# Kernel optimization log

Hardware: AMD Instinct MI355X
Metric: run time of the kernel (lower is better)

Reference implementation:

```python
import jax, jax.numpy as jnp
from jax import lax
import numpy as np

NODE = 100000
D = 256      # input_dim
H = 256      # hidden_dim
P = 4096     # num paths between the pair
L = 8        # path length (hops)
OUT = 1


def setup_inputs() -> dict:
    key = jax.random.key(0)
    ks = jax.random.split(key, 10)
    s = 1.0 / np.sqrt(H)
    return {
        "embedding": jax.random.normal(ks[0], (NODE, D), jnp.float32) * 0.1,
        "w_ih": jax.random.normal(ks[1], (4 * H, D), jnp.float32) * s,
        "w_hh": jax.random.normal(ks[2], (4 * H, H), jnp.float32) * s,
        "b_ih": jax.random.normal(ks[3], (4 * H,), jnp.float32) * s,
        "b_hh": jax.random.normal(ks[4], (4 * H,), jnp.float32) * s,
        "w_lin": jax.random.normal(ks[5], (OUT, H + 2 * D), jnp.float32) * 0.05,
        "b_lin": jax.random.normal(ks[6], (OUT,), jnp.float32) * 0.05,
        "paths": jax.random.randint(ks[7], (P, L), 0, NODE, jnp.int64),
        "user_id": jax.random.randint(ks[8], (1,), 0, NODE, jnp.int64),
        "item_id": jax.random.randint(ks[9], (1,), 0, NODE, jnp.int64),
    }


def _lstm_final_hidden(x, w_ih, w_hh, b_ih, b_hh):
    # x: [P, L, D] -> final hidden state h_n: [P, H] (PyTorch gate order i,f,g,o)
    p, _, _ = x.shape
    h = x.shape  # noqa (shape comment)
    hidden = w_hh.shape[1]
    b = b_ih + b_hh

    def step(carry, x_t):
        h, c = carry
        gates = x_t @ w_ih.T + h @ w_hh.T + b  # [P, 4H]
        i, f, g, o = jnp.split(gates, 4, axis=-1)
        c = jax.nn.sigmoid(f) * c + jax.nn.sigmoid(i) * jnp.tanh(g)
        h = jax.nn.sigmoid(o) * jnp.tanh(c)
        return (h, c), None

    h0 = jnp.zeros((p, hidden), x.dtype)
    c0 = jnp.zeros((p, hidden), x.dtype)
    (h_n, _), _ = lax.scan(step, (h0, c0), jnp.swapaxes(x, 0, 1))  # scan over L
    return h_n


def reference(embedding, w_ih, w_hh, b_ih, b_hh, w_lin, b_lin, paths, user_id, item_id):
    # Batched version of the per-path loop: embed all paths, one LSTM scan.
    x = embedding[paths]                                   # [P, L, D]
    sum_hidden = _lstm_final_hidden(x, w_ih, w_hh, b_ih, b_hh)  # [P, H] (== stacked h_n)

    # MaxPool2d((1, H)) over hidden dim -> attention logits over paths
    att = jnp.max(sum_hidden, axis=-1, keepdims=True)      # [P, 1]
    att = jax.nn.softmax(att, axis=0)                      # softmax over paths
    path_emb = jnp.sum(sum_hidden * att, axis=0, keepdims=True)  # [1, H]

    user_emb = embedding[user_id]                          # [1, D]
    item_emb = embedding[item_id]                          # [1, D]
    emb = jnp.concatenate([user_emb, item_emb, path_emb], axis=-1)  # [1, 2D+H]
    out = jax.nn.sigmoid(emb @ w_lin.T + b_lin)            # [1, OUT]
    return out
```

## Files before the change

kernel.cpp:

```cpp
#include <hip/hip_runtime.h>
#include <stdint.h>

#define NPATHS 4096
#define LPATH  8
#define DIM    256
#define HID    256

typedef short  short4v __attribute__((ext_vector_type(4)));
typedef short  short8v __attribute__((ext_vector_type(8)));
typedef float  float4v __attribute__((ext_vector_type(4)));

__device__ __forceinline__ unsigned short f2bf(float f) {
    union { float f; uint32_t u; } v; v.f = f;
    uint32_t u = v.u;
    u += 0x7FFFu + ((u >> 16) & 1u);
    return (unsigned short)(u >> 16);
}
__device__ __forceinline__ float bf2f(unsigned short s) {
    return __uint_as_float(((uint32_t)s) << 16);
}
__device__ __forceinline__ float fast_sigmoid(float x) {
    return 1.0f / (1.0f + __expf(-x));
}
__device__ __forceinline__ float fast_tanh(float x) {
    x = fminf(15.0f, fmaxf(-15.0f, x));
    float e = __expf(2.0f * x);
    return (e - 1.0f) / (e + 1.0f);
}

__device__ __forceinline__ void dma16(void* lds, const void* g) {
    typedef const unsigned int __attribute__((address_space(1)))* gp_t;
    typedef unsigned int __attribute__((address_space(3)))* lp_t;
    gp_t gp = reinterpret_cast<gp_t>(reinterpret_cast<uintptr_t>(g));
    lp_t lp = reinterpret_cast<lp_t>(static_cast<unsigned int>(reinterpret_cast<uintptr_t>(lds)));
    __builtin_amdgcn_global_load_lds(gp, lp, 16, 0, 0);
}

__global__ void prep_kernel(const float* __restrict__ w_ih, const float* __restrict__ w_hh,
                            const float* __restrict__ b_ih, const float* __restrict__ b_hh,
                            unsigned short* __restrict__ WfB, float* __restrict__ bias,
                            float* __restrict__ path_emb, unsigned int* __restrict__ done) {
    int gid  = blockIdx.x * 256 + threadIdx.x;
    int base = gid * 4;
    int j0   = base & 7;
    int unit = (base >> 3) & 255;
    int quad = (base >> 11) & 3;
    int gkc  = base >> 13;
    int g    = gkc >> 4, kc = gkc & 15;
    int row  = g * 256 + unit;
    int k    = kc * 32 + quad * 8 + j0;
    const float* src = (k < DIM) ? (w_ih + (size_t)row * DIM + k)
                                 : (w_hh + (size_t)row * HID + (k - DIM));
    float4 v = *(const float4*)src;
    short4v pk = {(short)f2bf(v.x), (short)f2bf(v.y), (short)f2bf(v.z), (short)f2bf(v.w)};
    *(short4v*)(WfB + base) = pk;
    if (gid < 1024) bias[gid] = b_ih[gid] + b_hh[gid];
    if (gid < 256)  path_emb[gid] = 0.0f;
    if (gid == 0)   *done = 0u;
}

__global__ __launch_bounds__(1024)
__attribute__((amdgpu_waves_per_eu(4, 4)))
void mega_kernel(const float* __restrict__ embedding, const int* __restrict__ paths,
                 const unsigned short* __restrict__ WfB, const float* __restrict__ bias,
                 unsigned short* __restrict__ h_final, float* __restrict__ logits) {
    __shared__ __align__(16) short sB[2][32768];
    __shared__ __align__(16) short sAx[8 * 512];
    __shared__ __align__(16) short h_lds[16 * 256];
    __shared__ float red[16 * 16];

    const int tid  = threadIdx.x;
    const int w    = tid >> 6;
    const int lane = tid & 63;
    const int l15  = lane & 15;
    const int quad = lane >> 4;
    const int p0   = blockIdx.x * 16;
    const int unit = w * 16 + l15;

    const int sg = w >> 2;
    const int sq = w & 3;
    const short* WfB_s = (const short*)WfB;

    auto stageB = [&](int kc, int slot) {
        const short* gsrc = WfB_s + (size_t)(sg * 16 + kc) * 8192 + sq * 2048 + lane * 8;
        short* ldst = &sB[slot][sg * 8192 + sq * 2048];
#pragma unroll
        for (int i = 0; i < 4; ++i)
            dma16(ldst + i * 512, gsrc + i * 512);
    };

    float bb[4];
#pragma unroll
    for (int g = 0; g < 4; ++g) bb[g] = bias[g * 256 + unit];

    const int grow = tid & 15;
    const int gk0  = (tid >> 4) * 4;
    const int gdst = (gk0 >> 5) * 512 + (((gk0 >> 3) & 3) * 16 + grow) * 8 + (gk0 & 4);
    {
        int node = paths[(p0 + grow) * LPATH];
        float4v v = __builtin_nontemporal_load(
            (const float4v*)(embedding + (size_t)node * DIM + gk0));
        short4v pk = {(short)f2bf(v[0]), (short)f2bf(v[1]),
                      (short)f2bf(v[2]), (short)f2bf(v[3])};
        *(short4v*)(&sAx[gdst]) = pk;
    }

    float cc[4] = {0.0f, 0.0f, 0.0f, 0.0f};

    stageB(0, 0);
    int cur = 0;
    __syncthreads();

#pragma unroll 1
    for (int t = 0; t < LPATH; ++t) {
        const bool first = (t == 0), last = (t == LPATH - 1);
        const int  K     = first ? 8 : 16;

        float4v gv;
        if (!last) {
            int node = paths[(p0 + grow) * LPATH + t + 1];
            gv = __builtin_nontemporal_load(
                (const float4v*)(embedding + (size_t)node * DIM + gk0));
        }

        float4v acc[4];
        const float4v z4 = {0.0f, 0.0f, 0.0f, 0.0f};
#pragma unroll
        for (int g = 0; g < 4; ++g) acc[g] = z4;

#pragma unroll 1
        for (int kc = 0; kc < K; ++kc) {
            int nxt = cur ^ 1;
            if (!(last && kc == K - 1))
                stageB((kc + 1 < K) ? kc + 1 : 0, nxt);

            short8v a;
            if (kc < 8) {
                a = *(const short8v*)(sAx + kc * 512 + lane * 8);
            } else {
                int cg  = (kc - 8) * 4 + quad;
                int cgs = cg ^ (l15 & 7);
                a = *(const short8v*)(&h_lds[l15 * 256 + cgs * 8]);
            }
#pragma unroll
            for (int g = 0; g < 4; ++g) {
                short8v bf = *(const short8v*)(&sB[cur][g * 8192 + quad * 2048 + unit * 8]);
                acc[g] = __builtin_amdgcn_mfma_f32_16x16x32_bf16(a, bf, acc[g], 0, 0, 0);
            }

            __syncthreads();
            cur = nxt;
        }

        if (!last) {
            short4v pk = {(short)f2bf(gv[0]), (short)f2bf(gv[1]),
                          (short)f2bf(gv[2]), (short)f2bf(gv[3])};
            *(short4v*)(&sAx[gdst]) = pk;
        }

        float hv[4];
#pragma unroll
        for (int r = 0; r < 4; ++r) {
            float iv = acc[0][r] + bb[0];
            float fv = acc[1][r] + bb[1];
            float gg = acc[2][r] + bb[2];
            float ov = acc[3][r] + bb[3];
            float cn = fast_sigmoid(fv) * cc[r] + fast_sigmoid(iv) * fast_tanh(gg);
            cc[r] = cn;
            hv[r] = fast_sigmoid(ov) * fast_tanh(cn);
        }

#pragma unroll
        for (int r = 0; r < 4; ++r) {
            int pr  = quad * 4 + r;
            int cgs = (unit >> 3) ^ (pr & 7);
            h_lds[pr * 256 + cgs * 8 + (unit & 7)] = (short)f2bf(hv[r]);
        }

        if (last) {
#pragma unroll
            for (int r = 0; r < 4; ++r) {
                float m = hv[r];
                m = fmaxf(m, __shfl_xor(m, 1, 64));
                m = fmaxf(m, __shfl_xor(m, 2, 64));
                m = fmaxf(m, __shfl_xor(m, 4, 64));
                m = fmaxf(m, __shfl_xor(m, 8, 64));
                if (l15 == 0) red[(quad * 4 + r) * 16 + w] = m;
            }
        }
        __syncthreads();
    }

    if (tid < 16) {
        float m = red[tid * 16];
#pragma unroll
        for (int j = 1; j < 16; ++j) m = fmaxf(m, red[tid * 16 + j]);
        logits[p0 + tid] = m;
    }
    if (tid < 512) {
        int row = tid >> 5, i5 = tid & 31;
        int cgs = i5 ^ (row & 7);
        short8v v = *(const short8v*)(&h_lds[row * 256 + cgs * 8]);
        *(short8v*)(h_final + (size_t)(p0 + row) * HID + (size_t)i5 * 8) = v;
    }
}

__global__ void attn_final_kernel(const unsigned short* __restrict__ h_final,
                                  const float* __restrict__ logits,
                                  float* __restrict__ path_emb,
                                  unsigned int* __restrict__ done,
                                  const float* __restrict__ embedding,
                                  const int* __restrict__ user_id,
                                  const int* __restrict__ item_id,
                                  const float* __restrict__ w_lin,
                                  const float* __restrict__ b_lin,
                                  float* __restrict__ out) {
    __shared__ float red[256];
    __shared__ float wts[16];
    __shared__ int lastf;
    int tid = threadIdx.x;
    int p0  = blockIdx.x * 16;

    float vals[16];
    float m = -1e30f;
#pragma unroll
    for (int i = 0; i < 16; ++i) {
        vals[i] = logits[i * 256 + tid];
        m = fmaxf(m, vals[i]);
    }
    red[tid] = m; __syncthreads();
    for (int s = 128; s > 0; s >>= 1) {
        if (tid < s) red[tid] = fmaxf(red[tid], red[tid + s]);
        __syncthreads();
    }
    m = red[0]; __syncthreads();
    float sum = 0.0f;
#pragma unroll
    for (int i = 0; i < 16; ++i) sum += __expf(vals[i] - m);
    red[tid] = sum; __syncthreads();
    for (int s = 128; s > 0; s >>= 1) {
        if (tid < s) red[tid] += red[tid + s];
        __syncthreads();
    }
    if (tid == 0) red[0] = 1.0f / red[0];
    __syncthreads();
    float invZ = red[0];
    if (tid < 16) wts[tid] = __expf(logits[p0 + tid] - m) * invZ;
    __syncthreads();

    float acc = 0.0f;
#pragma unroll
    for (int j = 0; j < 16; ++j)
        acc += wts[j] * bf2f(h_final[(size_t)(p0 + j) * HID + tid]);
    atomicAdd(&path_emb[tid], acc);

    __threadfence();
    __syncthreads();
    if (tid == 0) {
        unsigned int old = atomicAdd(done, 1u);
        lastf = (old == 255u) ? 1 : 0;
    }
    __syncthreads();
    if (lastf) {
        __threadfence();
        float pe = __hip_atomic_load(&path_emb[tid], __ATOMIC_RELAXED,
                                     __HIP_MEMORY_SCOPE_AGENT);
        int u  = user_id[0];
        int it = item_id[0];
        float s = w_lin[tid]       * embedding[(size_t)u  * DIM + tid]
                + w_lin[256 + tid] * embedding[(size_t)it * DIM + tid]
                + w_lin[512 + tid] * pe;
        red[tid] = s; __syncthreads();
        for (int st = 128; st > 0; st >>= 1) {
            if (tid < st) red[tid] += red[tid + st];
            __syncthreads();
        }
        if (tid == 0) out[0] = 1.0f / (1.0f + __expf(-(red[0] + b_lin[0])));
    }
}

extern "C" void kernel_launch(void* const* d_in, const int* in_sizes, int n_in,
                              void* d_out, int out_size, void* d_ws, size_t ws_size,
                              hipStream_t stream) {
    const float* embedding = (const float*)d_in[0];
    const float* w_ih      = (const float*)d_in[1];
    const float* w_hh      = (const float*)d_in[2];
    const float* b_ih      = (const float*)d_in[3];
    const float* b_hh      = (const float*)d_in[4];
    const float* w_lin     = (const float*)d_in[5];
    const float* b_lin     = (const float*)d_in[6];
    const int*   paths     = (const int*)d_in[7];
    const int*   user_id   = (const int*)d_in[8];
    const int*   item_id   = (const int*)d_in[9];
    float* outp = (float*)d_out;

    char* ws = (char*)d_ws;
    size_t off = 0;
    auto alloc = [&](size_t n) { void* p = ws + off; off = (off + n + 255) & ~(size_t)255; return p; };
    unsigned short* WfB      = (unsigned short*)alloc((size_t)1024 * 512 * 2);
    float*          bias     = (float*)alloc(1024 * 4);
    float*          path_emb = (float*)alloc(HID * 4);
    float*          logits   = (float*)alloc(NPATHS * 4);
    unsigned short* h_final  = (unsigned short*)alloc((size_t)NPATHS * HID * 2);
    unsigned int*   done     = (unsigned int*)alloc(4);

    prep_kernel<<<512, 256, 0, stream>>>(w_ih, w_hh, b_ih, b_hh, WfB, bias,
                                         path_emb, done);

    mega_kernel<<<256, 1024, 0, stream>>>(embedding, paths, WfB, bias,
                                          h_final, logits);

    attn_final_kernel<<<256, 256, 0, stream>>>(h_final, logits, path_emb, done,
                                               embedding, user_id, item_id,
                                               w_lin, b_lin, outp);
}
```

Before: 280.6 us.

## Load LSTM weight fragments directly from global instead of LDS double-buffering

Removes the double-buffered LDS staging of the bf16 weight matrix via global_load_lds, along with the per-k-chunk barrier. Each wave now reads its weight fragments straight from global memory (L2-resident) into registers for the MFMAs. This drops 128KB of LDS use and one __syncthreads per k-chunk, leaving one barrier per timestep. In exchange, each of the 256 blocks streams the full weight matrix from L2 on every step with no latency hiding, so per-k-chunk global load latency is exposed.

```diff
diff --git a/kernel.cpp b/kernel.cpp
--- a/kernel.cpp
+++ b/kernel.cpp
@@ -26,14 +26,6 @@
     x = fminf(15.0f, fmaxf(-15.0f, x));
     float e = __expf(2.0f * x);
     return (e - 1.0f) / (e + 1.0f);
-}
-
-__device__ __forceinline__ void dma16(void* lds, const void* g) {
-    typedef const unsigned int __attribute__((address_space(1)))* gp_t;
-    typedef unsigned int __attribute__((address_space(3)))* lp_t;
-    gp_t gp = reinterpret_cast<gp_t>(reinterpret_cast<uintptr_t>(g));
-    lp_t lp = reinterpret_cast<lp_t>(static_cast<unsigned int>(reinterpret_cast<uintptr_t>(lds)));
-    __builtin_amdgcn_global_load_lds(gp, lp, 16, 0, 0);
 }
 
 __global__ void prep_kernel(const float* __restrict__ w_ih, const float* __restrict__ w_hh,
@@ -64,7 +56,6 @@
 void mega_kernel(const float* __restrict__ embedding, const int* __restrict__ paths,
                  const unsigned short* __restrict__ WfB, const float* __restrict__ bias,
                  unsigned short* __restrict__ h_final, float* __restrict__ logits) {
-    __shared__ __align__(16) short sB[2][32768];
     __shared__ __align__(16) short sAx[8 * 512];
     __shared__ __align__(16) short h_lds[16 * 256];
     __shared__ float red[16 * 16];
@@ -77,17 +68,7 @@
     const int p0   = blockIdx.x * 16;
     const int unit = w * 16 + l15;
 
-    const int sg = w >> 2;
-    const int sq = w & 3;
-    const short* WfB_s = (const short*)WfB;
-
-    auto stageB = [&](int kc, int slot) {
-        const short* gsrc = WfB_s + (size_t)(sg * 16 + kc) * 8192 + sq * 2048 + lane * 8;
-        short* ldst = &sB[slot][sg * 8192 + sq * 2048];
-#pragma unroll
-        for (int i = 0; i < 4; ++i)
-            dma16(ldst + i * 512, gsrc + i * 512);
-    };
+    const short* bb0 = (const short*)WfB + quad * 2048 + unit * 8;
 
     float bb[4];
 #pragma unroll
@@ -107,8 +88,6 @@
 
     float cc[4] = {0.0f, 0.0f, 0.0f, 0.0f};
 
-    stageB(0, 0);
-    int cur = 0;
     __syncthreads();
 
 #pragma unroll 1
@@ -130,10 +109,6 @@
 
 #pragma unroll 1
         for (int kc = 0; kc < K; ++kc) {
-            int nxt = cur ^ 1;
-            if (!(last && kc == K - 1))
-                stageB((kc + 1 < K) ? kc + 1 : 0, nxt);
-
             short8v a;
             if (kc < 8) {
                 a = *(const short8v*)(sAx + kc * 512 + lane * 8);
@@ -142,15 +117,18 @@
                 int cgs = cg ^ (l15 & 7);
                 a = *(const short8v*)(&h_lds[l15 * 256 + cgs * 8]);
             }
-#pragma unroll
-            for (int g = 0; g < 4; ++g) {
-                short8v bf = *(const short8v*)(&sB[cur][g * 8192 + quad * 2048 + unit * 8]);
-                acc[g] = __builtin_amdgcn_mfma_f32_16x16x32_bf16(a, bf, acc[g], 0, 0, 0);
-            }
-
-            __syncthreads();
-            cur = nxt;
-        }
+            const short* bk = bb0 + kc * 8192;
+            short8v bf0 = *(const short8v*)(bk);
+            short8v bf1 = *(const short8v*)(bk + 131072);
+            short8v bf2 = *(const short8v*)(bk + 262144);
+            short8v bf3 = *(const short8v*)(bk + 393216);
+            acc[0] = __builtin_amdgcn_mfma_f32_16x16x32_bf16(a, bf0, acc[0], 0, 0, 0);
+            acc[1] = __builtin_amdgcn_mfma_f32_16x16x32_bf16(a, bf1, acc[1], 0, 0, 0);
+            acc[2] = __builtin_amdgcn_mfma_f32_16x16x32_bf16(a, bf2, acc[2], 0, 0, 0);
+            acc[3] = __builtin_amdgcn_mfma_f32_16x16x32_bf16(a, bf3, acc[3], 0, 0, 0);
+        }
+
+        __syncthreads();
 
         if (!last) {
             short4v pk = {(short)f2bf(gv[0]), (short)f2bf(gv[1]),
```

New measurement: 259.2 us. -7.6%, faster.
